# Kernel tuning notes

Measured on AMD Instinct MI355X. Metric: run time of the kernel, lower is better.

## Reference

```python
import math
import jax, jax.numpy as jnp
import numpy as np

B, H, L = 8, 512, 4096
N = 64 // 2  # d_state//2 complex pairs
DT_MIN, DT_MAX = 1e-3, 0.1


def setup_inputs() -> dict:
    key = jax.random.key(0)
    k_u, k_dt, k_C, k_D, k_W = jax.random.split(key, 5)
    u = jax.random.normal(k_u, (B, H, L), dtype=jnp.float32)
    log_dt = jax.random.uniform(k_dt, (H,), dtype=jnp.float32) * (
        math.log(DT_MAX) - math.log(DT_MIN)) + math.log(DT_MIN)
    log_A_real = jnp.log(0.5 * jnp.ones((H, N), dtype=jnp.float32))
    A_imag = math.pi * jnp.broadcast_to(jnp.arange(N, dtype=jnp.float32), (H, N))
    C = jax.random.normal(k_C, (H, N, 2), dtype=jnp.float32)  # view_as_real of cfloat
    D = jax.random.normal(k_D, (H,), dtype=jnp.float32)
    W_out = jax.random.normal(k_W, (2 * H, H), dtype=jnp.float32) * 0.05  # 1x1 conv weight
    b_out = jnp.zeros((2 * H,), dtype=jnp.float32)
    return {"u": u, "log_dt": log_dt, "log_A_real": log_A_real, "A_imag": A_imag,
            "C": C, "D": D, "W_out": W_out, "b_out": b_out}


def _ssm_kernel(log_dt, log_A_real, A_imag, C, length):
    dt = jnp.exp(log_dt)                             # (H,)
    A = -jnp.exp(log_A_real) + 1j * A_imag           # (H,N) complex
    dtA = A * dt[:, None]                            # (H,N)
    l = jnp.arange(length, dtype=jnp.float32)
    K = jnp.exp(dtA[:, :, None] * l)                 # (H,N,L) complex Vandermonde
    Cc = C[..., 0] + 1j * C[..., 1]                  # (H,N)
    Cs = Cc * (jnp.exp(dtA) - 1.0) / A               # (H,N)
    return 2.0 * jnp.einsum('hn,hnl->hl', Cs, K).real  # (H,L) real kernel


def reference(u, log_dt, log_A_real, A_imag, C, D, W_out, b_out):
    length = u.shape[-1]
    k = _ssm_kernel(log_dt, log_A_real, A_imag, C, length)  # (H,L)
    n_fft = 2 * length
    k_f = jnp.fft.rfft(k, n=n_fft)                   # (H, L+1)
    u_f = jnp.fft.rfft(u, n=n_fft)                   # (B,H,L+1)
    y = jnp.fft.irfft(u_f * k_f, n=n_fft)[..., :length]  # FFT convolution
    y = y + u * D[:, None]                           # D skip connection
    y = jax.nn.gelu(y, approximate=False)            # torch nn.GELU = exact erf
    y = jnp.einsum('oh,bhl->bol', W_out, y) + b_out[:, None]  # 1x1 conv
    a, b = jnp.split(y, 2, axis=-2)                  # GLU over channel dim
    return a * jax.nn.sigmoid(b)
```

## Files before the change

### kernel.cpp

```cpp
#include <hip/hip_runtime.h>
#include <math.h>

constexpr int cB = 8, cH = 512, cL = 4096, cN = 32;
constexpr int cG = 32, cLC = 128;
constexpr int cHN = cH * cN;

constexpr size_t OF_RR  = 0;
constexpr size_t OF_RI  = (size_t)cHN;
constexpr size_t OF_RPR = (size_t)2*cHN;
constexpr size_t OF_RPI = (size_t)3*cHN;
constexpr size_t OF_C2R = (size_t)4*cHN;
constexpr size_t OF_C2I = (size_t)5*cHN;
constexpr size_t OF_DR  = (size_t)6*cHN;
constexpr size_t OF_DI  = (size_t)7*cHN;
constexpr size_t OF_K   = (size_t)8*cHN;
constexpr size_t OF_WP  = OF_K + (size_t)512*128;
constexpr size_t OF_A   = OF_WP + (size_t)1024*512/2;
constexpr size_t OF_V   = OF_A + (size_t)512*128*192/2;
constexpr size_t OF_XP  = OF_V + (size_t)512*64*128/2;
constexpr size_t OF_G   = OF_XP + (size_t)512*256*64/2;
constexpr size_t OF_GT  = OF_A;

typedef __bf16 bf16x8 __attribute__((ext_vector_type(8)));
typedef float  f32x4  __attribute__((ext_vector_type(4)));

static __device__ __forceinline__ ushort f2bf(float x) {
    unsigned u = __float_as_uint(x);
    unsigned r = (u + 0x7fffu + ((u >> 16) & 1u)) >> 16;
    return (ushort)r;
}
static __device__ __forceinline__ float bf2f(ushort v) {
    return __uint_as_float(((unsigned)v) << 16);
}
static __device__ __forceinline__ unsigned pk2(float a, float b) {
    return (unsigned)f2bf(a) | ((unsigned)f2bf(b) << 16);
}
static __device__ __forceinline__ float gelu(float v) {
    return 0.5f * v * (1.0f + erff(v * 0.70710678118654752f));
}
static __device__ __forceinline__ void gload16(const void* g, void* l) {
    __builtin_amdgcn_global_load_lds(
        (const __attribute__((address_space(1))) unsigned*)g,
        (__attribute__((address_space(3))) unsigned*)l, 16, 0, 0);
}

__global__ void k_consts_vmat(const float* __restrict__ log_dt,
                              const float* __restrict__ log_A_real,
                              const float* __restrict__ A_imag,
                              const float* __restrict__ Cin,
                              float* __restrict__ ws,
                              ushort* __restrict__ wsu)
{
    int tid = blockIdx.x * 256 + threadIdx.x;
    if (tid >= cHN) return;
    int h = tid >> 5, n = tid & 31;
    float dt = expf(log_dt[h]);
    float Ar = -expf(log_A_real[tid]);
    float Ai = A_imag[tid];
    float dr = dt * Ar, di = dt * Ai;
    float er = expf(dr);
    float rr = er * cosf(di), ri = er * sinf(di);
    float erL = expf(dr * (float)cLC);
    float diL = di * (float)cLC;
    float rpr = erL * cosf(diL), rpi = erL * sinf(diL);
    float cr = Cin[2*tid], ci = Cin[2*tid+1];
    float nr = rr - 1.0f, ni = ri;
    float inv = 1.0f / (Ar*Ar + Ai*Ai);
    float wr = (nr*Ar + ni*Ai) * inv;
    float wi = (ni*Ar - nr*Ai) * inv;
    float csr = cr*wr - ci*wi;
    float csi = cr*wi + ci*wr;
    ws[OF_RR  + tid] = rr;  ws[OF_RI  + tid] = ri;
    ws[OF_RPR + tid] = rpr; ws[OF_RPI + tid] = rpi;
    ws[OF_C2R + tid] = 2.0f*csr; ws[OF_C2I + tid] = 2.0f*csi;
    ws[OF_DR  + tid] = dr;  ws[OF_DI  + tid] = di;

    float e127 = expf(dr * 127.f), a127 = di * 127.f;
    float pr = e127 * cosf(a127), pi_ = e127 * sinf(a127);
    float rie = expf(-dr);
    float rc = rie * cosf(di), rs = -rie * sinf(di);
    ushort* vre = wsu + 2*OF_V + ((size_t)h*64 + n) * 128;
    ushort* vim = wsu + 2*OF_V + ((size_t)h*64 + 32 + n) * 128;
    for (int j4 = 0; j4 < 128; j4 += 4) {
        ushort4 r4, i4;
        #pragma unroll
        for (int e = 0; e < 4; ++e) {
            ((ushort*)&r4)[e] = f2bf(pr);
            ((ushort*)&i4)[e] = f2bf(pi_);
            float npr = pr*rc - pi_*rs;
            float npi = pr*rs + pi_*rc;
            pr = npr; pi_ = npi;
        }
        *(ushort4*)&vre[j4] = r4;
        *(ushort4*)&vim[j4] = i4;
    }
}

__global__ void k_pack_w(const float* __restrict__ W, ushort* __restrict__ Wp)
{
    int idx = blockIdx.x * 256 + threadIdx.x;
    int base = idx * 4;
    int m = base >> 9;
    int k = base & 511;
    int src = (m & 1) ? (512 + (m >> 1)) : (m >> 1);
    float4 v = *(const float4*)&W[(size_t)src * 512 + k];
    ushort4 o;
    o.x = f2bf(v.x); o.y = f2bf(v.y); o.z = f2bf(v.z); o.w = f2bf(v.w);
    *(ushort4*)&Wp[base] = o;
}

__global__ void k_embt(const float* __restrict__ ws, const float* __restrict__ Dvec,
                       ushort* __restrict__ wsu)
{
    __shared__ float kv[256];
    int t = threadIdx.x;
    int tid = blockIdx.x * 256 + t;
    int h = tid >> 7, l = tid & 127;
    float fl = (float)l, fl1 = (float)(l + 1);
    const float* dr_ = ws + OF_DR + (size_t)h*32;
    const float* di_ = ws + OF_DI + (size_t)h*32;
    const float* c2r_ = ws + OF_C2R + (size_t)h*32;
    const float* c2i_ = ws + OF_C2I + (size_t)h*32;
    ushort* rowA = wsu + 2*OF_A + ((size_t)h*128 + l) * 192;
    float kacc = 0.f;
    for (int n4 = 0; n4 < 32; n4 += 4) {
        ushort4 prq, npq;
        #pragma unroll
        for (int e = 0; e < 4; ++e) {
            int n = n4 + e;
            float dr = dr_[n], di = di_[n], c2r = c2r_[n], c2i = c2i_[n];
            float e0 = expf(dr * fl), a0 = di * fl;
            float c0 = cosf(a0), s0 = sinf(a0);
            kacc += e0 * (c2r*c0 - c2i*s0);
            float e1 = expf(dr * fl1), a1 = di * fl1;
            float c1 = cosf(a1), s1 = sinf(a1);
            ((ushort*)&prq)[e] = f2bf(e1 * (c2r*c1 - c2i*s1));
            ((ushort*)&npq)[e] = f2bf(-e1 * (c2r*s1 + c2i*c1));
        }
        *(ushort4*)&rowA[128 + n4] = prq;
        *(ushort4*)&rowA[160 + n4] = npq;
    }
    kv[t] = kacc;
    __syncthreads();
    const float* krow = kv + ((t >> 7) << 7);
    float Dh = Dvec[h];
    for (int j8 = 0; j8 < 128; j8 += 8) {
        uint4 q;
        unsigned w[4];
        #pragma unroll
        for (int p = 0; p < 4; ++p) {
            int j0 = j8 + 2*p, j1 = j0 + 1;
            float v0 = (j0 <= l) ? krow[l - j0] : 0.f;
            float v1 = (j1 <= l) ? krow[l - j1] : 0.f;
            if (j0 == l) v0 += Dh;
            if (j1 == l) v1 += Dh;
            w[p] = pk2(v0, v1);
        }
        q.x = w[0]; q.y = w[1]; q.z = w[2]; q.w = w[3];
        *(uint4*)&rowA[j8] = q;
    }
}

__global__ __launch_bounds__(256) void k_state_gemm(const float* __restrict__ u,
                                                    const ushort* __restrict__ wsu,
                                                    ushort* __restrict__ xp)
{
    __shared__ ushort Vs[64 * 136];
    __shared__ ushort Bs[256 * 40];
    const int t = threadIdx.x;
    const int h = blockIdx.x;
    const int wn = t >> 6, lane = t & 63;
    const int lm = lane & 15, q = lane >> 4;

    {
        int idx = t * 32;
        int row = idx >> 7, kk = idx & 127;
        const ushort* src = wsu + 2*OF_V + ((size_t)h*64 + row) * 128 + kk;
        uint4 v0 = *(const uint4*)&src[0],  v1 = *(const uint4*)&src[8];
        uint4 v2 = *(const uint4*)&src[16], v3 = *(const uint4*)&src[24];
        ushort* d = (ushort*)Vs + row * 136 + kk;
        *(uint4*)&d[0] = v0; *(uint4*)&d[8] = v1;
        *(uint4*)&d[16] = v2; *(uint4*)&d[24] = v3;
    }

    const int b = t >> 5, c = t & 31;
    f32x4 acc[4][4];
    #pragma unroll
    for (int i = 0; i < 4; ++i)
        #pragma unroll
        for (int j = 0; j < 4; ++j) acc[i][j] = (f32x4){0.f,0.f,0.f,0.f};

    for (int k0 = 0; k0 < 128; k0 += 32) {
        const float* up = u + ((size_t)(b*cH + h)) * cL + (size_t)c*128 + k0;
        float4 f[8];
        #pragma unroll
        for (int e = 0; e < 8; ++e) f[e] = *(const float4*)&up[4*e];
        __syncthreads();
        ushort* d = (ushort*)Bs + t * 40;
        #pragma unroll
        for (int e = 0; e < 4; ++e) {
            uint4 w;
            w.x = pk2(f[2*e].x, f[2*e].y);   w.y = pk2(f[2*e].z, f[2*e].w);
            w.z = pk2(f[2*e+1].x, f[2*e+1].y); w.w = pk2(f[2*e+1].z, f[2*e+1].w);
            *(uint4*)&d[8*e] = w;
        }
        __syncthreads();
        bf16x8 af[4], bfr[4];
        #pragma unroll
        for (int mi = 0; mi < 4; ++mi)
            af[mi] = *(const bf16x8*)&Vs[(16*mi + lm) * 136 + k0 + 8*q];
        #pragma unroll
        for (int ni = 0; ni < 4; ++ni)
            bfr[ni] = *(const bf16x8*)&Bs[(64*wn + 16*ni + lm) * 40 + 8*q];
        #pragma unroll
        for (int mi = 0; mi < 4; ++mi)
            #pragma unroll
            for (int ni = 0; ni < 4; ++ni)
                acc[mi][ni] = __builtin_amdgcn_mfma_f32_16x16x32_bf16(af[mi], bfr[ni], acc[mi][ni], 0,0,0);
    }
    #pragma unroll
    for (int mi = 0; mi < 4; ++mi)
        #pragma unroll
        for (int ni = 0; ni < 4; ++ni) {
            int col = 64*wn + 16*ni + lm;
            int comp = 16*mi + 4*q;
            ushort4 st;
            st.x = f2bf(acc[mi][ni][0]); st.y = f2bf(acc[mi][ni][1]);
            st.z = f2bf(acc[mi][ni][2]); st.w = f2bf(acc[mi][ni][3]);
            *(ushort4*)&xp[((size_t)h*256 + col) * 64 + comp] = st;
        }
}

__global__ __launch_bounds__(256) void k_scan2(const float* __restrict__ ws,
                                               ushort* __restrict__ xp)
{
    int tid = blockIdx.x * 256 + threadIdx.x;
    int n  = tid & 31;
    int bh = tid >> 5;
    int h  = bh & (cH - 1);
    int b  = bh >> 9;
    float rpr = ws[OF_RPR + (size_t)h*32 + n];
    float rpi = ws[OF_RPI + (size_t)h*32 + n];
    float Xr = 0.f, Xi = 0.f;
    ushort* base = xp + ((size_t)h*256 + (size_t)b*32) * 64 + n;
    for (int c = 0; c < cG; ++c) {
        ushort* p = base + (size_t)c * 64;
        float sr = bf2f(p[0]), si = bf2f(p[32]);
        p[0]  = f2bf(Xr);
        p[32] = f2bf(Xi);
        float nXr = fmaf(rpr, Xr, fmaf(-rpi, Xi, sr));
        float nXi = fmaf(rpr, Xi, fmaf(rpi, Xr, si));
        Xr = nXr; Xi = nXi;
    }
}

__global__ __launch_bounds__(512) void k_conv(const float* __restrict__ u,
                                              const ushort* __restrict__ wsu,
                                              ushort* __restrict__ g)
{
    __shared__ ushort As[128 * 200];
    __shared__ ushort Bs[256 * 200];
    const int t = threadIdx.x;
    const int h = blockIdx.x;
    const int wave = t >> 6, lane = t & 63;
    const int wm = wave & 1, wn = wave >> 1;
    const int lm = lane & 15, q = lane >> 4;

    {
        const int row = t >> 2, c0 = (t & 3) * 48;
        const ushort* Ab = wsu + 2*OF_A + ((size_t)h*128 + row) * 192 + c0;
        ushort* d = &As[row * 200 + c0];
        #pragma unroll
        for (int e = 0; e < 6; ++e)
            *(uint4*)&d[8*e] = *(const uint4*)&Ab[8*e];
    }
    {
        const int gc = t >> 1, half = t & 1;
        const int ub = gc >> 5, uc = gc & 31;
        const float* up = u + ((size_t)(ub*cH + h)) * cL + (size_t)uc*128 + half*64;
        ushort* d = &Bs[gc * 200 + half*64];
        #pragma unroll
        for (int e = 0; e < 8; ++e) {
            float4 f0 = *(const float4*)&up[8*e];
            float4 f1 = *(const float4*)&up[8*e + 4];
            uint4 w;
            w.x = pk2(f0.x, f0.y); w.y = pk2(f0.z, f0.w);
            w.z = pk2(f1.x, f1.y); w.w = pk2(f1.z, f1.w);
            *(uint4*)&d[8*e] = w;
        }
        const ushort* xs = wsu + 2*OF_XP + ((size_t)h*256 + gc) * 64 + half*32;
        ushort* dx = &Bs[gc * 200 + 128 + half*32];
        #pragma unroll
        for (int e = 0; e < 4; ++e)
            *(uint4*)&dx[8*e] = *(const uint4*)&xs[8*e];
    }
    __syncthreads();

    f32x4 acc[4][4];
    #pragma unroll
    for (int i = 0; i < 4; ++i)
        #pragma unroll
        for (int j = 0; j < 4; ++j) acc[i][j] = (f32x4){0.f,0.f,0.f,0.f};

    #pragma unroll
    for (int k0 = 0; k0 < 192; k0 += 32) {
        if ((wm == 0) && (k0 == 64 || k0 == 96)) continue;
        bf16x8 af[4], bfr[4];
        #pragma unroll
        for (int mi = 0; mi < 4; ++mi)
            af[mi] = *(const bf16x8*)&As[(64*wm + 16*mi + lm) * 200 + k0 + 8*q];
        #pragma unroll
        for (int ni = 0; ni < 4; ++ni)
            bfr[ni] = *(const bf16x8*)&Bs[(64*wn + 16*ni + lm) * 200 + k0 + 8*q];
        #pragma unroll
        for (int mi = 0; mi < 4; ++mi)
            #pragma unroll
            for (int ni = 0; ni < 4; ++ni)
                acc[mi][ni] = __builtin_amdgcn_mfma_f32_16x16x32_bf16(af[mi], bfr[ni], acc[mi][ni], 0,0,0);
    }
    #pragma unroll
    for (int ni = 0; ni < 4; ++ni) {
        int gc = 64*wn + 16*ni + lm;
        int ob = gc >> 5, oc = gc & 31;
        ushort* grow = g + ((size_t)(ob*cH + h)) * cL + (size_t)oc*128;
        #pragma unroll
        for (int mi = 0; mi < 4; ++mi) {
            int l = 64*wm + 16*mi + 4*q;
            ushort4 st;
            st.x = f2bf(gelu(acc[mi][ni][0]));
            st.y = f2bf(gelu(acc[mi][ni][1]));
            st.z = f2bf(gelu(acc[mi][ni][2]));
            st.w = f2bf(gelu(acc[mi][ni][3]));
            *(ushort4*)&grow[l] = st;
        }
    }
}

__global__ __launch_bounds__(256) void k_transpose(const ushort* __restrict__ gsrc,
                                                   ushort* __restrict__ gT)
{
    __shared__ ushort tile[64 * 64];
    const int t = threadIdx.x;
    const int b  = blockIdx.z;
    const int h0 = blockIdx.y << 6;
    const int l0 = blockIdx.x << 6;
    const ushort* gb = gsrc + ((size_t)b * cH + h0) * cL + l0;
    const int lb = t & 7;
    #pragma unroll
    for (int half = 0; half < 2; ++half) {
        int r = (t >> 3) + half * 32;
        uint4 v = *(const uint4*)&gb[(size_t)r * cL + lb * 8];
        int sb = lb ^ (r & 7) ^ (r >> 3);
        *(uint4*)&tile[r * 64 + sb * 8] = v;
    }
    __syncthreads();
    ushort* gTb = gT + ((size_t)b * cL + l0) * cH + h0;
    #pragma unroll
    for (int half = 0; half < 2; ++half) {
        int l  = (t >> 3) + half * 32;
        int hb = t & 7;
        ushort vals[8];
        #pragma unroll
        for (int e = 0; e < 8; ++e) {
            int r  = hb * 8 + e;
            int sb = (l >> 3) ^ (r & 7) ^ (r >> 3);
            vals[e] = tile[r * 64 + sb * 8 + (l & 7)];
        }
        *(uint4*)&gTb[(size_t)l * cH + hb * 8] = *(uint4*)vals;
    }
}

__global__ __launch_bounds__(256) void k_gemm2(const ushort* __restrict__ Wp,
                                               const float* __restrict__ bias,
                                               const ushort* __restrict__ gT,
                                               float* __restrict__ out)
{
    __shared__ ushort As[2][128 * 32];
    __shared__ ushort Bs[2][128 * 32];
    const int t    = threadIdx.x;
    const int l0   = blockIdx.x * 128;
    const int by   = blockIdx.y;
    const int b    = blockIdx.z;
    const int wave = t >> 6, lane = t & 63;
    const int wm   = wave & 1, wn = wave >> 1;
    const int lm   = lane & 15, q = lane >> 4;

    const int srow = lane >> 2;
    const int scol = (lane & 3) * 8;
    const ushort* Ag = Wp + (size_t)(by * 128) * 512;
    const ushort* Bg = gT + ((size_t)b * cL + l0) * 512;

    f32x4 acc[4][4];
    #pragma unroll
    for (int i = 0; i < 4; ++i)
        #pragma unroll
        for (int j = 0; j < 4; ++j)
            acc[i][j] = (f32x4){0.f, 0.f, 0.f, 0.f};

    auto stage = [&](ushort* Asb, ushort* Bsb, int k0) {
        #pragma unroll
        for (int j = 0; j < 2; ++j) {
            int row = 32*wave + 16*j + srow;
            gload16(Ag + (size_t)row * 512 + k0 + scol,
                    (char*)Asb + wave*2048 + j*1024);
            gload16(Bg + (size_t)row * 512 + k0 + scol,
                    (char*)Bsb + wave*2048 + j*1024);
        }
    };
    auto compute = [&](const ushort* Asb, const ushort* Bsb) {
        bf16x8 af[4], bfr[4];
        #pragma unroll
        for (int mi = 0; mi < 4; ++mi)
            af[mi] = *(const bf16x8*)&Asb[(64*wm + 16*mi + lm) * 32 + 8*q];
        #pragma unroll
        for (int ni = 0; ni < 4; ++ni)
            bfr[ni] = *(const bf16x8*)&Bsb[(64*wn + 16*ni + lm) * 32 + 8*q];
        #pragma unroll
        for (int mi = 0; mi < 4; ++mi)
            #pragma unroll
            for (int ni = 0; ni < 4; ++ni)
                acc[mi][ni] = __builtin_amdgcn_mfma_f32_16x16x32_bf16(af[mi], bfr[ni], acc[mi][ni], 0,0,0);
    };

    stage(As[0], Bs[0], 0);
    __syncthreads();
    int cur = 0;
    for (int ks = 0; ks < 15; ++ks) {
        stage(As[cur ^ 1], Bs[cur ^ 1], (ks + 1) * 32);
        compute(As[cur], Bs[cur]);
        __syncthreads();
        cur ^= 1;
    }
    compute(As[cur], Bs[cur]);

    const int obase = by * 64 + 32 * wm;
    #pragma unroll
    for (int mi = 0; mi < 4; ++mi) {
        #pragma unroll
        for (int p = 0; p < 2; ++p) {
            int o = obase + 8*mi + 2*q + p;
            float ba = bias[o], bb = bias[512 + o];
            float* orow = out + ((size_t)b * cH + o) * cL + l0 + 64*wn + lm;
            #pragma unroll
            for (int ni = 0; ni < 4; ++ni) {
                float av = acc[mi][ni][2*p]     + ba;
                float gv = acc[mi][ni][2*p + 1] + bb;
                orow[16 * ni] = av / (1.f + expf(-gv));
            }
        }
    }
}

extern "C" void kernel_launch(void* const* d_in, const int* in_sizes, int n_in,
                              void* d_out, int out_size, void* d_ws, size_t ws_size,
                              hipStream_t stream)
{
    (void)in_sizes; (void)n_in; (void)out_size; (void)ws_size;
    const float* u          = (const float*)d_in[0];
    const float* log_dt     = (const float*)d_in[1];
    const float* log_A_real = (const float*)d_in[2];
    const float* A_imag     = (const float*)d_in[3];
    const float* C          = (const float*)d_in[4];
    const float* D          = (const float*)d_in[5];
    const float* W          = (const float*)d_in[6];
    const float* bias       = (const float*)d_in[7];
    float* out = (float*)d_out;
    float* ws  = (float*)d_ws;
    ushort* wsu = (ushort*)d_ws;
    ushort* Wp  = wsu + 2*OF_WP;
    ushort* xp  = wsu + 2*OF_XP;
    ushort* gbf = wsu + 2*OF_G;
    ushort* gTu = wsu + 2*OF_GT;

    hipLaunchKernelGGL(k_consts_vmat, dim3(cHN/256), dim3(256), 0, stream,
                       log_dt, log_A_real, A_imag, C, ws, wsu);
    hipLaunchKernelGGL(k_pack_w, dim3(1024*512/4/256), dim3(256), 0, stream, W, Wp);
    hipLaunchKernelGGL(k_embt, dim3(512*128/256), dim3(256), 0, stream, ws, D, wsu);
    hipLaunchKernelGGL(k_state_gemm, dim3(512), dim3(256), 0, stream, u, wsu, xp);
    hipLaunchKernelGGL(k_scan2, dim3(cB*cH*cN/256), dim3(256), 0, stream, ws, xp);
    hipLaunchKernelGGL(k_conv, dim3(512), dim3(512), 0, stream, u, wsu, gbf);
    hipLaunchKernelGGL(k_transpose, dim3(cL/64, cH/64, cB), dim3(256), 0, stream, gbf, gTu);
    hipLaunchKernelGGL(k_gemm2, dim3(cL/128, 1024/128, cB), dim3(256), 0, stream,
                       Wp, bias, gTu, out);
}
```

Before: 282.9 us.

## Fuse chunk-state scan into conv kernel and cache bf16 input from state GEMM

The state GEMM now also writes a bf16 copy of u into the g buffer, so the conv kernel reads half-width input instead of reloading and converting fp32 u. The separate k_scan2 launch is removed, and the sequential scan over chunk states now runs in shared memory inside k_conv before its MFMA loop. This cuts one kernel launch and reduces global traffic for u. In exchange it adds a serial scan phase in which only half the threads work while the others wait at the barrier. Because k_conv reads ubf and writes g in the same buffer, correctness depends on each block only overwriting the region it has already loaded.

```diff
diff --git a/kernel.cpp b/kernel.cpp
--- a/kernel.cpp
+++ b/kernel.cpp
@@ -163,7 +163,8 @@
 
 __global__ __launch_bounds__(256) void k_state_gemm(const float* __restrict__ u,
                                                     const ushort* __restrict__ wsu,
-                                                    ushort* __restrict__ xp)
+                                                    ushort* __restrict__ xp,
+                                                    ushort* __restrict__ ubf)
 {
     __shared__ ushort Vs[64 * 136];
     __shared__ ushort Bs[256 * 40];
@@ -195,15 +196,23 @@
         float4 f[8];
         #pragma unroll
         for (int e = 0; e < 8; ++e) f[e] = *(const float4*)&up[4*e];
+        uint4 w[4];
+        #pragma unroll
+        for (int e = 0; e < 4; ++e) {
+            w[e].x = pk2(f[2*e].x, f[2*e].y);     w[e].y = pk2(f[2*e].z, f[2*e].w);
+            w[e].z = pk2(f[2*e+1].x, f[2*e+1].y); w[e].w = pk2(f[2*e+1].z, f[2*e+1].w);
+        }
+        {
+            ushort* ub_row = ubf + ((size_t)(b*cH + h)) * cL + (size_t)c*128 + k0;
+            #pragma unroll
+            for (int e = 0; e < 4; ++e)
+                *(uint4*)&ub_row[8*e] = w[e];
+        }
         __syncthreads();
         ushort* d = (ushort*)Bs + t * 40;
         #pragma unroll
-        for (int e = 0; e < 4; ++e) {
-            uint4 w;
-            w.x = pk2(f[2*e].x, f[2*e].y);   w.y = pk2(f[2*e].z, f[2*e].w);
-            w.z = pk2(f[2*e+1].x, f[2*e+1].y); w.w = pk2(f[2*e+1].z, f[2*e+1].w);
-            *(uint4*)&d[8*e] = w;
-        }
+        for (int e = 0; e < 4; ++e)
+            *(uint4*)&d[8*e] = w[e];
         __syncthreads();
         bf16x8 af[4], bfr[4];
         #pragma unroll
@@ -231,32 +240,10 @@
         }
 }
 
-__global__ __launch_bounds__(256) void k_scan2(const float* __restrict__ ws,
-                                               ushort* __restrict__ xp)
-{
-    int tid = blockIdx.x * 256 + threadIdx.x;
-    int n  = tid & 31;
-    int bh = tid >> 5;
-    int h  = bh & (cH - 1);
-    int b  = bh >> 9;
-    float rpr = ws[OF_RPR + (size_t)h*32 + n];
-    float rpi = ws[OF_RPI + (size_t)h*32 + n];
-    float Xr = 0.f, Xi = 0.f;
-    ushort* base = xp + ((size_t)h*256 + (size_t)b*32) * 64 + n;
-    for (int c = 0; c < cG; ++c) {
-        ushort* p = base + (size_t)c * 64;
-        float sr = bf2f(p[0]), si = bf2f(p[32]);
-        p[0]  = f2bf(Xr);
-        p[32] = f2bf(Xi);
-        float nXr = fmaf(rpr, Xr, fmaf(-rpi, Xi, sr));
-        float nXi = fmaf(rpr, Xi, fmaf(rpi, Xr, si));
-        Xr = nXr; Xi = nXi;
-    }
-}
-
-__global__ __launch_bounds__(512) void k_conv(const float* __restrict__ u,
+__global__ __launch_bounds__(512) void k_conv(const ushort* ubf,
+                                              const float* __restrict__ ws,
                                               const ushort* __restrict__ wsu,
-                                              ushort* __restrict__ g)
+                                              ushort* g)
 {
     __shared__ ushort As[128 * 200];
     __shared__ ushort Bs[256 * 200];
@@ -277,22 +264,34 @@
     {
         const int gc = t >> 1, half = t & 1;
         const int ub = gc >> 5, uc = gc & 31;
-        const float* up = u + ((size_t)(ub*cH + h)) * cL + (size_t)uc*128 + half*64;
+        const ushort* up = ubf + ((size_t)(ub*cH + h)) * cL + (size_t)uc*128 + half*64;
         ushort* d = &Bs[gc * 200 + half*64];
         #pragma unroll
-        for (int e = 0; e < 8; ++e) {
-            float4 f0 = *(const float4*)&up[8*e];
-            float4 f1 = *(const float4*)&up[8*e + 4];
-            uint4 w;
-            w.x = pk2(f0.x, f0.y); w.y = pk2(f0.z, f0.w);
-            w.z = pk2(f1.x, f1.y); w.w = pk2(f1.z, f1.w);
-            *(uint4*)&d[8*e] = w;
-        }
+        for (int e = 0; e < 8; ++e)
+            *(uint4*)&d[8*e] = *(const uint4*)&up[8*e];
         const ushort* xs = wsu + 2*OF_XP + ((size_t)h*256 + gc) * 64 + half*32;
         ushort* dx = &Bs[gc * 200 + 128 + half*32];
         #pragma unroll
         for (int e = 0; e < 4; ++e)
             *(uint4*)&dx[8*e] = *(const uint4*)&xs[8*e];
+    }
+    __syncthreads();
+
+    if (t < 256) {
+        const int sb = t >> 5, sn = t & 31;
+        float rpr = ws[OF_RPR + (size_t)h*32 + sn];
+        float rpi = ws[OF_RPI + (size_t)h*32 + sn];
+        float Xr = 0.f, Xi = 0.f;
+        ushort* p = &Bs[(sb*32) * 200 + 128 + sn];
+        #pragma unroll 4
+        for (int c = 0; c < cG; ++c, p += 200) {
+            float sr = bf2f(p[0]), si = bf2f(p[32]);
+            p[0]  = f2bf(Xr);
+            p[32] = f2bf(Xi);
+            float nXr = fmaf(rpr, Xr, fmaf(-rpi, Xi, sr));
+            float nXi = fmaf(rpr, Xi, fmaf(rpi, Xr, si));
+            Xr = nXr; Xi = nXi;
+        }
     }
     __syncthreads();
 
@@ -476,9 +475,8 @@
                        log_dt, log_A_real, A_imag, C, ws, wsu);
     hipLaunchKernelGGL(k_pack_w, dim3(1024*512/4/256), dim3(256), 0, stream, W, Wp);
     hipLaunchKernelGGL(k_embt, dim3(512*128/256), dim3(256), 0, stream, ws, D, wsu);
-    hipLaunchKernelGGL(k_state_gemm, dim3(512), dim3(256), 0, stream, u, wsu, xp);
-    hipLaunchKernelGGL(k_scan2, dim3(cB*cH*cN/256), dim3(256), 0, stream, ws, xp);
-    hipLaunchKernelGGL(k_conv, dim3(512), dim3(512), 0, stream, u, wsu, gbf);
+    hipLaunchKernelGGL(k_state_gemm, dim3(512), dim3(256), 0, stream, u, wsu, xp, gbf);
+    hipLaunchKernelGGL(k_conv, dim3(512), dim3(512), 0, stream, gbf, ws, wsu, gbf);
     hipLaunchKernelGGL(k_transpose, dim3(cL/64, cH/64, cB), dim3(256), 0, stream, gbf, gTu);
     hipLaunchKernelGGL(k_gemm2, dim3(cL/128, 1024/128, cB), dim3(256), 0, stream,
                        Wp, bias, gTu, out);
```

Result: slower. 290.9 us (+2.8%).

## Fuse state GEMM and chunk scan into conv kernel via shared memory

Applied to the files above, without the earlier changes.

Moves the per-chunk state GEMM (V times u chunks) and the sequential complex scan across chunks into the k_conv kernel. Results stay in shared memory (the Bs columns 128..191) instead of going through the xp global buffer, and two kernel launches are removed. The As staging is deferred through registers so the V matrix can temporarily occupy As. This saves a second read of u, the xp round trips and launch gaps, but serializes the scan on half the threads inside each block and adds register pressure.

```diff
diff --git a/kernel.cpp b/kernel.cpp
--- a/kernel.cpp
+++ b/kernel.cpp
@@ -161,100 +161,8 @@
     }
 }
 
-__global__ __launch_bounds__(256) void k_state_gemm(const float* __restrict__ u,
-                                                    const ushort* __restrict__ wsu,
-                                                    ushort* __restrict__ xp)
-{
-    __shared__ ushort Vs[64 * 136];
-    __shared__ ushort Bs[256 * 40];
-    const int t = threadIdx.x;
-    const int h = blockIdx.x;
-    const int wn = t >> 6, lane = t & 63;
-    const int lm = lane & 15, q = lane >> 4;
-
-    {
-        int idx = t * 32;
-        int row = idx >> 7, kk = idx & 127;
-        const ushort* src = wsu + 2*OF_V + ((size_t)h*64 + row) * 128 + kk;
-        uint4 v0 = *(const uint4*)&src[0],  v1 = *(const uint4*)&src[8];
-        uint4 v2 = *(const uint4*)&src[16], v3 = *(const uint4*)&src[24];
-        ushort* d = (ushort*)Vs + row * 136 + kk;
-        *(uint4*)&d[0] = v0; *(uint4*)&d[8] = v1;
-        *(uint4*)&d[16] = v2; *(uint4*)&d[24] = v3;
-    }
-
-    const int b = t >> 5, c = t & 31;
-    f32x4 acc[4][4];
-    #pragma unroll
-    for (int i = 0; i < 4; ++i)
-        #pragma unroll
-        for (int j = 0; j < 4; ++j) acc[i][j] = (f32x4){0.f,0.f,0.f,0.f};
-
-    for (int k0 = 0; k0 < 128; k0 += 32) {
-        const float* up = u + ((size_t)(b*cH + h)) * cL + (size_t)c*128 + k0;
-        float4 f[8];
-        #pragma unroll
-        for (int e = 0; e < 8; ++e) f[e] = *(const float4*)&up[4*e];
-        __syncthreads();
-        ushort* d = (ushort*)Bs + t * 40;
-        #pragma unroll
-        for (int e = 0; e < 4; ++e) {
-            uint4 w;
-            w.x = pk2(f[2*e].x, f[2*e].y);   w.y = pk2(f[2*e].z, f[2*e].w);
-            w.z = pk2(f[2*e+1].x, f[2*e+1].y); w.w = pk2(f[2*e+1].z, f[2*e+1].w);
-            *(uint4*)&d[8*e] = w;
-        }
-        __syncthreads();
-        bf16x8 af[4], bfr[4];
-        #pragma unroll
-        for (int mi = 0; mi < 4; ++mi)
-            af[mi] = *(const bf16x8*)&Vs[(16*mi + lm) * 136 + k0 + 8*q];
-        #pragma unroll
-        for (int ni = 0; ni < 4; ++ni)
-            bfr[ni] = *(const bf16x8*)&Bs[(64*wn + 16*ni + lm) * 40 + 8*q];
-        #pragma unroll
-        for (int mi = 0; mi < 4; ++mi)
-            #pragma unroll
-            for (int ni = 0; ni < 4; ++ni)
-                acc[mi][ni] = __builtin_amdgcn_mfma_f32_16x16x32_bf16(af[mi], bfr[ni], acc[mi][ni], 0,0,0);
-    }
-    #pragma unroll
-    for (int mi = 0; mi < 4; ++mi)
-        #pragma unroll
-        for (int ni = 0; ni < 4; ++ni) {
-            int col = 64*wn + 16*ni + lm;
-            int comp = 16*mi + 4*q;
-            ushort4 st;
-            st.x = f2bf(acc[mi][ni][0]); st.y = f2bf(acc[mi][ni][1]);
-            st.z = f2bf(acc[mi][ni][2]); st.w = f2bf(acc[mi][ni][3]);
-            *(ushort4*)&xp[((size_t)h*256 + col) * 64 + comp] = st;
-        }
-}
-
-__global__ __launch_bounds__(256) void k_scan2(const float* __restrict__ ws,
-                                               ushort* __restrict__ xp)
-{
-    int tid = blockIdx.x * 256 + threadIdx.x;
-    int n  = tid & 31;
-    int bh = tid >> 5;
-    int h  = bh & (cH - 1);
-    int b  = bh >> 9;
-    float rpr = ws[OF_RPR + (size_t)h*32 + n];
-    float rpi = ws[OF_RPI + (size_t)h*32 + n];
-    float Xr = 0.f, Xi = 0.f;
-    ushort* base = xp + ((size_t)h*256 + (size_t)b*32) * 64 + n;
-    for (int c = 0; c < cG; ++c) {
-        ushort* p = base + (size_t)c * 64;
-        float sr = bf2f(p[0]), si = bf2f(p[32]);
-        p[0]  = f2bf(Xr);
-        p[32] = f2bf(Xi);
-        float nXr = fmaf(rpr, Xr, fmaf(-rpi, Xi, sr));
-        float nXi = fmaf(rpr, Xi, fmaf(rpi, Xr, si));
-        Xr = nXr; Xi = nXi;
-    }
-}
-
 __global__ __launch_bounds__(512) void k_conv(const float* __restrict__ u,
+                                              const float* __restrict__ ws,
                                               const ushort* __restrict__ wsu,
                                               ushort* __restrict__ g)
 {
@@ -266,13 +174,19 @@
     const int wm = wave & 1, wn = wave >> 1;
     const int lm = lane & 15, q = lane >> 4;
 
+    uint4 areg[6];
+    const int arow = t >> 2, ac0 = (t & 3) * 48;
     {
-        const int row = t >> 2, c0 = (t & 3) * 48;
-        const ushort* Ab = wsu + 2*OF_A + ((size_t)h*128 + row) * 192 + c0;
-        ushort* d = &As[row * 200 + c0];
-        #pragma unroll
-        for (int e = 0; e < 6; ++e)
-            *(uint4*)&d[8*e] = *(const uint4*)&Ab[8*e];
+        const ushort* Ab = wsu + 2*OF_A + ((size_t)h*128 + arow) * 192 + ac0;
+        #pragma unroll
+        for (int e = 0; e < 6; ++e) areg[e] = *(const uint4*)&Ab[8*e];
+    }
+    {
+        const int vrow = t >> 3, vc0 = (t & 7) * 16;
+        const ushort* vs = wsu + 2*OF_V + ((size_t)h*64 + vrow) * 128 + vc0;
+        uint4 v0 = *(const uint4*)&vs[0], v1 = *(const uint4*)&vs[8];
+        *(uint4*)&As[vrow*200 + vc0]     = v0;
+        *(uint4*)&As[vrow*200 + vc0 + 8] = v1;
     }
     {
         const int gc = t >> 1, half = t & 1;
@@ -288,11 +202,63 @@
             w.z = pk2(f1.x, f1.y); w.w = pk2(f1.z, f1.w);
             *(uint4*)&d[8*e] = w;
         }
-        const ushort* xs = wsu + 2*OF_XP + ((size_t)h*256 + gc) * 64 + half*32;
-        ushort* dx = &Bs[gc * 200 + 128 + half*32];
-        #pragma unroll
-        for (int e = 0; e < 4; ++e)
-            *(uint4*)&dx[8*e] = *(const uint4*)&xs[8*e];
+    }
+    __syncthreads();
+
+    {
+        f32x4 accs[4][2];
+        #pragma unroll
+        for (int i = 0; i < 4; ++i)
+            #pragma unroll
+            for (int j = 0; j < 2; ++j) accs[i][j] = (f32x4){0.f,0.f,0.f,0.f};
+        #pragma unroll
+        for (int j0 = 0; j0 < 128; j0 += 32) {
+            bf16x8 vf[4], uf[2];
+            #pragma unroll
+            for (int mi = 0; mi < 4; ++mi)
+                vf[mi] = *(const bf16x8*)&As[(16*mi + lm) * 200 + j0 + 8*q];
+            #pragma unroll
+            for (int ni = 0; ni < 2; ++ni)
+                uf[ni] = *(const bf16x8*)&Bs[(32*wave + 16*ni + lm) * 200 + j0 + 8*q];
+            #pragma unroll
+            for (int mi = 0; mi < 4; ++mi)
+                #pragma unroll
+                for (int ni = 0; ni < 2; ++ni)
+                    accs[mi][ni] = __builtin_amdgcn_mfma_f32_16x16x32_bf16(vf[mi], uf[ni], accs[mi][ni], 0,0,0);
+        }
+        #pragma unroll
+        for (int mi = 0; mi < 4; ++mi)
+            #pragma unroll
+            for (int ni = 0; ni < 2; ++ni) {
+                int col = 32*wave + 16*ni + lm;
+                ushort4 st;
+                st.x = f2bf(accs[mi][ni][0]); st.y = f2bf(accs[mi][ni][1]);
+                st.z = f2bf(accs[mi][ni][2]); st.w = f2bf(accs[mi][ni][3]);
+                *(ushort4*)&Bs[col*200 + 128 + 16*mi + 4*q] = st;
+            }
+    }
+    __syncthreads();
+
+    if (t < 256) {
+        const int sb = t >> 5, sn = t & 31;
+        float rpr = ws[OF_RPR + (size_t)h*32 + sn];
+        float rpi = ws[OF_RPI + (size_t)h*32 + sn];
+        float Xr = 0.f, Xi = 0.f;
+        ushort* p = &Bs[(sb*32) * 200 + 128 + sn];
+        #pragma unroll 4
+        for (int c = 0; c < cG; ++c, p += 200) {
+            float sr = bf2f(p[0]), si = bf2f(p[32]);
+            p[0]  = f2bf(Xr);
+            p[32] = f2bf(Xi);
+            float nXr = fmaf(rpr, Xr, fmaf(-rpi, Xi, sr));
+            float nXi = fmaf(rpr, Xi, fmaf(rpi, Xr, si));
+            Xr = nXr; Xi = nXi;
+        }
+    }
+    {
+        ushort* d = &As[arow*200 + ac0];
+        #pragma unroll
+        for (int e = 0; e < 6; ++e) *(uint4*)&d[8*e] = areg[e];
     }
     __syncthreads();
 
@@ -468,7 +434,6 @@
     float* ws  = (float*)d_ws;
     ushort* wsu = (ushort*)d_ws;
     ushort* Wp  = wsu + 2*OF_WP;
-    ushort* xp  = wsu + 2*OF_XP;
     ushort* gbf = wsu + 2*OF_G;
     ushort* gTu = wsu + 2*OF_GT;
 
@@ -476,9 +441,7 @@
                        log_dt, log_A_real, A_imag, C, ws, wsu);
     hipLaunchKernelGGL(k_pack_w, dim3(1024*512/4/256), dim3(256), 0, stream, W, Wp);
     hipLaunchKernelGGL(k_embt, dim3(512*128/256), dim3(256), 0, stream, ws, D, wsu);
-    hipLaunchKernelGGL(k_state_gemm, dim3(512), dim3(256), 0, stream, u, wsu, xp);
-    hipLaunchKernelGGL(k_scan2, dim3(cB*cH*cN/256), dim3(256), 0, stream, ws, xp);
-    hipLaunchKernelGGL(k_conv, dim3(512), dim3(512), 0, stream, u, wsu, gbf);
+    hipLaunchKernelGGL(k_conv, dim3(512), dim3(512), 0, stream, u, ws, wsu, gbf);
     hipLaunchKernelGGL(k_transpose, dim3(cL/64, cH/64, cB), dim3(256), 0, stream, gbf, gTu);
     hipLaunchKernelGGL(k_gemm2, dim3(cL/128, 1024/128, cB), dim3(256), 0, stream,
                        Wp, bias, gTu, out);
```

Result: faster. 267.2 us (-5.5%).
